# Kernel tuning notes

Hardware: AMD Instinct MI355X
Metric: run time of the kernel (lower is better)

Reference implementation:

```python
import jax, jax.numpy as jnp
import numpy as np

RES = 32            # input grid resolution
OUT_RES = 64        # after subdivide
C = 128             # channels (== out_channels -> skip is identity)
G = 32              # group-norm groups
N = 8192            # active input voxels
EPS = 1e-5

# 8 child offsets for subdivide, 27 stencil offsets for 3x3x3 submanifold conv
_OFFS8 = np.stack(np.meshgrid([0, 1], [0, 1], [0, 1], indexing='ij'), -1).reshape(-1, 3).astype(np.int32)
_OFFS27 = np.stack(np.meshgrid([-1, 0, 1], [-1, 0, 1], [-1, 0, 1], indexing='ij'), -1).reshape(-1, 3).astype(np.int32)


def group_norm(x, gamma, beta, num_groups=G, eps=EPS):
    # sparse group norm over all active voxels of the (single) sample
    n, c = x.shape
    xg = x.reshape(n, num_groups, c // num_groups)
    mean = xg.mean(axis=(0, 2), keepdims=True)
    var = xg.var(axis=(0, 2), keepdims=True)
    xn = (xg - mean) * jax.lax.rsqrt(var + eps)
    return xn.reshape(n, c) * gamma + beta


def subdivide_coords(coords):
    offs = jnp.asarray(_OFFS8)
    return (coords[:, None, :] * 2 + offs[None, :, :]).reshape(-1, 3)  # [8N, 3]


def subm_conv3d(feats, coords, W, b, grid_res):
    # submanifold 3x3x3 sparse conv: outputs only at active sites
    n = feats.shape[0]
    grid = jnp.full((grid_res, grid_res, grid_res), -1, dtype=jnp.int32)
    grid = grid.at[coords[:, 0], coords[:, 1], coords[:, 2]].set(
        jnp.arange(n, dtype=jnp.int32))
    out = jnp.zeros((n, W.shape[-1]), dtype=feats.dtype)
    for k in range(27):  # fixed small stencil loop
        off = jnp.asarray(_OFFS27[k])
        nb = coords + off
        inb = jnp.all((nb >= 0) & (nb < grid_res), axis=1)
        nbc = jnp.clip(nb, 0, grid_res - 1)
        idx = grid[nbc[:, 0], nbc[:, 1], nbc[:, 2]]
        mask = inb & (idx >= 0)
        g = jnp.where(mask[:, None], feats[jnp.where(mask, idx, 0)], 0.0)
        out = out + g @ W[k]
    return out + b


def setup_inputs() -> dict:
    key = jax.random.key(0)
    ks = jax.random.split(key, 8)
    rng = np.random.default_rng(0)
    flat = rng.choice(RES ** 3, size=N, replace=False)
    coords = np.stack([flat // (RES * RES), (flat // RES) % RES, flat % RES],
                      axis=-1).astype(np.int32)
    feats = jax.random.normal(ks[0], (N, C), dtype=jnp.float32)
    gamma1 = 1.0 + 0.1 * jax.random.normal(ks[1], (C,), dtype=jnp.float32)
    beta1 = 0.1 * jax.random.normal(ks[2], (C,), dtype=jnp.float32)
    W1 = jax.random.normal(ks[3], (27, C, C), dtype=jnp.float32) * 0.05
    b1 = jax.random.normal(ks[4], (C,), dtype=jnp.float32) * 0.05
    gamma2 = 1.0 + 0.1 * jax.random.normal(ks[5], (C,), dtype=jnp.float32)
    beta2 = 0.1 * jax.random.normal(ks[6], (C,), dtype=jnp.float32)
    W2 = jax.random.normal(ks[7], (27, C, C), dtype=jnp.float32) * 0.05
    b2 = jax.random.normal(jax.random.fold_in(key, 99), (C,), dtype=jnp.float32) * 0.05
    return {"feats": feats, "gamma1": gamma1, "beta1": beta1, "W1": W1,
            "b1": b1, "gamma2": gamma2, "beta2": beta2, "W2": W2, "b2": b2,
            "coords": jnp.asarray(coords)}


def reference(feats, gamma1, beta1, W1, b1, gamma2, beta2, W2, b2, coords):
    # act_layers: GroupNorm + SiLU at input resolution
    h = jax.nn.silu(group_norm(feats, gamma1, beta1))
    # subdivide both branch and residual (8 children per voxel)
    new_coords = subdivide_coords(coords)          # [8N, 3] in OUT_RES grid
    h = jnp.repeat(h, 8, axis=0)
    x_sub = jnp.repeat(feats, 8, axis=0)
    # out_layers: conv3 -> GN -> SiLU -> conv3 (submanifold, same active set)
    h = subm_conv3d(h, new_coords, W1, b1, OUT_RES)
    h = jax.nn.silu(group_norm(h, gamma2, beta2))
    h = subm_conv3d(h, new_coords, W2, b2, OUT_RES)
    # skip_connection is Identity since out_channels == channels
    return h + x_sub
```

## Files before the change

### kernel.cpp

```cpp
#include <hip/hip_runtime.h>

#define NPAR   8192
#define NCH    65536
#define RES    32
#define EPS    1e-5f

typedef __attribute__((ext_vector_type(8))) short short8;
typedef __attribute__((ext_vector_type(4))) float floatx4;

__device__ __forceinline__ unsigned short f2bf(float f) {
    union { float f; unsigned u; } v; v.f = f;
    unsigned r = v.u + 0x7fffu + ((v.u >> 16) & 1u);
    return (unsigned short)(r >> 16);
}
__device__ __forceinline__ float bf2f(unsigned short b) {
    union { unsigned u; float f; } v; v.u = ((unsigned)b) << 16;
    return v.f;
}
__device__ __forceinline__ void glds16(const void* g, void* l) {
    __builtin_amdgcn_global_load_lds(
        (__attribute__((address_space(1))) const void*)g,
        (__attribute__((address_space(3))) void*)l, 16, 0, 0);
}
__device__ __forceinline__ int k27_of(int o, int s) {
    return (((o >> 2) & 1) + ((s >> 2) & 1)) * 9 +
           (((o >> 1) & 1) + ((s >> 1) & 1)) * 3 +
           ((o & 1) + (s & 1));
}
__device__ __forceinline__ void axis_dlist(int o, int s, int* d, int& n) {
    if (o == 0) { if (s == 0) { d[0] = -1; n = 1; } else { d[0] = 0; d[1] = 1; n = 2; } }
    else        { if (s == 0) { d[0] = -1; d[1] = 0; n = 2; } else { d[0] = 1; n = 1; } }
}

__global__ void k1_kernel(const int* __restrict__ coords, int* __restrict__ grid32,
                          const float* __restrict__ x, float* __restrict__ sum,
                          float* __restrict__ sq) {
    int b = blockIdx.x;
    int t = threadIdx.x;
    if (b < 32) {
        int p = b * 256 + t;
        grid32[(coords[p*3] << 10) + (coords[p*3+1] << 5) + coords[p*3+2]] = p;
    } else {
        __shared__ float s_sum[32], s_sq[32];
        if (t < 32) { s_sum[t] = 0.0f; s_sq[t] = 0.0f; }
        __syncthreads();
        const float4* x4 = (const float4*)x;
        int total = NPAR * 32;
        int idx0 = (b - 32) * 256 + t;
        int g = idx0 & 31;
        float ls = 0.0f, lq = 0.0f;
        for (int idx = idx0; idx < total; idx += 256 * 256) {
            float4 v = x4[idx];
            ls += v.x + v.y + v.z + v.w;
            lq += v.x * v.x + v.y * v.y + v.z * v.z + v.w * v.w;
        }
        atomicAdd(&s_sum[g], ls);
        atomicAdd(&s_sq[g], lq);
        __syncthreads();
        if (t < 32) { atomicAdd(&sum[t], s_sum[t]); atomicAdd(&sq[t], s_sq[t]); }
    }
}

__global__ void k2_kernel(const int* __restrict__ coords, const int* __restrict__ grid32,
                          int* __restrict__ idx_tab, int* __restrict__ pidx27,
                          const float* __restrict__ W1, const float* __restrict__ W2,
                          unsigned short* __restrict__ Wc1f, unsigned short* __restrict__ Wp2,
                          const float* __restrict__ x, const float* __restrict__ sum,
                          const float* __restrict__ sq, const float* __restrict__ gamma,
                          const float* __restrict__ beta, unsigned short* __restrict__ y) {
    int b = blockIdx.x;
    if (b < 32) {
        int p = b * 256 + threadIdx.x;
        int cx = coords[p*3], cy = coords[p*3+1], cz = coords[p*3+2];
        int r27[27];
#pragma unroll
        for (int k = 0; k < 27; ++k) {
            int nx = cx + k / 9 - 1, ny = cy + (k / 3) % 3 - 1, nz = cz + k % 3 - 1;
            int r = -1;
            if ((unsigned)nx < 32u && (unsigned)ny < 32u && (unsigned)nz < 32u) {
                int g = grid32[(nx << 10) + (ny << 5) + nz];
                if ((unsigned)g < (unsigned)NPAR) r = g;
            }
            r27[k] = r;
            pidx27[k * NPAR + p] = r;
        }
#pragma unroll
        for (int k = 0; k < 27; ++k) {
            const int dx = k / 9 - 1, dy = (k / 3) % 3 - 1, dz = k % 3 - 1;
            int v[8];
#pragma unroll
            for (int o = 0; o < 8; ++o) {
                const int ex = ((o >> 2) & 1) + dx;
                const int ey = ((o >> 1) & 1) + dy;
                const int ez = (o & 1) + dz;
                const int ptap = ((ex >> 1) + 1) * 9 + ((ey >> 1) + 1) * 3 + ((ez >> 1) + 1);
                const int slot = ((ex & 1) << 2) + ((ey & 1) << 1) + (ez & 1);
                int r = r27[ptap];
                v[o] = (r >= 0) ? slot * NPAR + r : -1;
            }
            int4* dst = (int4*)&idx_tab[k * NCH + p * 8];
            dst[0] = make_int4(v[0], v[1], v[2], v[3]);
            dst[1] = make_int4(v[4], v[5], v[6], v[7]);
        }
    } else if (b < 248) {
        int rem = (b - 32) * 256 + threadIdx.x;
        int lane = rem & 63;
        int ks   = (rem >> 6) & 3;
        int nb   = (rem >> 8) & 7;
        int tap  = rem >> 11;
        int n  = nb * 16 + (lane & 15);
        int k0 = ks * 32 + (lane >> 4) * 8;
        unsigned short v[8];
#pragma unroll
        for (int j = 0; j < 8; ++j) v[j] = f2bf(W2[tap * 16384 + (k0 + j) * 128 + n]);
        uint4 pk;
        pk.x = (unsigned)v[0] | ((unsigned)v[1] << 16);
        pk.y = (unsigned)v[2] | ((unsigned)v[3] << 16);
        pk.z = (unsigned)v[4] | ((unsigned)v[5] << 16);
        pk.w = (unsigned)v[6] | ((unsigned)v[7] << 16);
        *(uint4*)&Wp2[(long)rem * 8] = pk;
    } else if (b < 760) {
        int rem = (b - 248) * 256 + threadIdx.x;
        int lane  = rem & 63;
        int ks    = (rem >> 6) & 3;
        int nb    = (rem >> 8) & 7;
        int combo = rem >> 11;
        int o = combo >> 3, s = combo & 7;
        int n  = nb * 16 + (lane & 15);
        int k0 = ks * 32 + (lane >> 4) * 8;
        int d0[2], d1[2], d2[2], n0, n1, n2;
        axis_dlist((o >> 2) & 1, (s >> 2) & 1, d0, n0);
        axis_dlist((o >> 1) & 1, (s >> 1) & 1, d1, n1);
        axis_dlist(o & 1,        s & 1,        d2, n2);
        unsigned short v[8];
#pragma unroll
        for (int j = 0; j < 8; ++j) {
            float acc = 0.0f;
            for (int a = 0; a < n0; ++a)
                for (int bb = 0; bb < n1; ++bb)
                    for (int cc = 0; cc < n2; ++cc) {
                        int kk = (d0[a] + 1) * 9 + (d1[bb] + 1) * 3 + (d2[cc] + 1);
                        acc += W1[kk * 16384 + (k0 + j) * 128 + n];
                    }
            v[j] = f2bf(acc);
        }
        uint4 pk;
        pk.x = (unsigned)v[0] | ((unsigned)v[1] << 16);
        pk.y = (unsigned)v[2] | ((unsigned)v[3] << 16);
        pk.z = (unsigned)v[4] | ((unsigned)v[5] << 16);
        pk.w = (unsigned)v[6] | ((unsigned)v[7] << 16);
        *(uint4*)&Wc1f[(long)rem * 8] = pk;
    } else {
        const float4* x4 = (const float4*)x;
        uint2* y2 = (uint2*)y;
        const float4* g4 = (const float4*)gamma;
        const float4* b4 = (const float4*)beta;
        float cnt = (float)NPAR * 4.0f;
        int total = NPAR * 32;
        for (int idx = (b - 760) * 256 + threadIdx.x; idx < total; idx += 256 * 256) {
            int c4 = idx & 31;
            float mean = sum[c4] / cnt;
            float var = sq[c4] / cnt - mean * mean;
            float rstd = rsqrtf(var + EPS);
            float4 v = x4[idx];
            float4 gm = g4[c4];
            float4 bt = b4[c4];
            float a[4] = {v.x, v.y, v.z, v.w};
            float gg[4] = {gm.x, gm.y, gm.z, gm.w};
            float bb[4] = {bt.x, bt.y, bt.z, bt.w};
            unsigned short o[4];
#pragma unroll
            for (int i = 0; i < 4; ++i) {
                float tv = (a[i] - mean) * rstd * gg[i] + bb[i];
                o[i] = f2bf(tv / (1.0f + __expf(-tv)));
            }
            uint2 pk;
            pk.x = (unsigned)o[0] | ((unsigned)o[1] << 16);
            pk.y = (unsigned)o[2] | ((unsigned)o[3] << 16);
            y2[idx] = pk;
        }
    }
}

__global__ void gn_apply_bf16_kernel(unsigned short* __restrict__ x,
                                     const float* __restrict__ sum, const float* __restrict__ sq,
                                     const float* __restrict__ gamma, const float* __restrict__ beta,
                                     int nrows) {
    uint2* x2 = (uint2*)x;
    const float4* g4 = (const float4*)gamma;
    const float4* b4 = (const float4*)beta;
    float cnt = (float)nrows * 4.0f;
    int total = nrows * 32;
    for (int idx = blockIdx.x * blockDim.x + threadIdx.x; idx < total;
         idx += gridDim.x * blockDim.x) {
        int c4 = idx & 31;
        float mean = sum[c4] / cnt;
        float var = sq[c4] / cnt - mean * mean;
        float rstd = rsqrtf(var + EPS);
        uint2 pk = x2[idx];
        float a[4] = {bf2f((unsigned short)(pk.x & 0xffff)), bf2f((unsigned short)(pk.x >> 16)),
                      bf2f((unsigned short)(pk.y & 0xffff)), bf2f((unsigned short)(pk.y >> 16))};
        float4 gm = g4[c4];
        float4 bt = b4[c4];
        float gg[4] = {gm.x, gm.y, gm.z, gm.w};
        float bb[4] = {bt.x, bt.y, bt.z, bt.w};
        unsigned short o[4];
#pragma unroll
        for (int i = 0; i < 4; ++i) {
            float tv = (a[i] - mean) * rstd * gg[i] + bb[i];
            o[i] = f2bf(tv / (1.0f + __expf(-tv)));
        }
        pk.x = (unsigned)o[0] | ((unsigned)o[1] << 16);
        pk.y = (unsigned)o[2] | ((unsigned)o[3] << 16);
        x2[idx] = pk;
    }
}

__device__ __forceinline__ void mfma_phase(
    const unsigned short* __restrict__ Abuf, short8 (&bfr)[2][4],
    floatx4 (&acc)[8][2], int aswz) {
#pragma unroll
    for (int ks = 0; ks < 4; ++ks) {
        short8 afr[8];
#pragma unroll
        for (int mt = 0; mt < 8; ++mt)
            afr[mt] = *(const short8*)&Abuf[(mt << 11) + (ks << 9) + aswz];
#pragma unroll
        for (int mt = 0; mt < 8; ++mt)
#pragma unroll
            for (int nt = 0; nt < 2; ++nt)
                acc[mt][nt] = __builtin_amdgcn_mfma_f32_16x16x32_bf16(
                    afr[mt], bfr[nt][ks], acc[mt][nt], 0, 0, 0);
    }
}
__device__ __forceinline__ void loadB(const unsigned short* __restrict__ Wtap,
                                      short8 (&bfr)[2][4], int wn, int lane) {
#pragma unroll
    for (int nt = 0; nt < 2; ++nt)
#pragma unroll
        for (int ks = 0; ks < 4; ++ks)
            bfr[nt][ks] = *(const short8*)&Wtap[(((wn * 2 + nt) << 2) + ks) * 512 + (lane << 3)];
}
__device__ __forceinline__ void stageA(const unsigned short* __restrict__ Ag,
                                       int iv0, int iv1, const unsigned short* zsrc,
                                       unsigned short* __restrict__ buf,
                                       int base0, int base1, int cchOff) {
    const unsigned short* g0 = (iv0 >= 0) ? Ag + (long)iv0 * 128 : zsrc;
    const unsigned short* g1 = (iv1 >= 0) ? Ag + (long)iv1 * 128 : zsrc;
#pragma unroll
    for (int i = 0; i < 4; ++i) glds16(g0 + i * 32 + cchOff, &buf[base0 + i * 512]);
#pragma unroll
    for (int i = 0; i < 4; ++i) glds16(g1 + i * 32 + cchOff, &buf[base1 + i * 512]);
}

__global__ void __launch_bounds__(256, 2) conv1_fold_kernel(
    const unsigned short* __restrict__ Ag, const unsigned short* __restrict__ Wc1f,
    const float* __restrict__ bias, const int* __restrict__ pidx27,
    unsigned short* __restrict__ outp, const float* __restrict__ zpage,
    float* __restrict__ gsum, float* __restrict__ gsq) {
    __shared__ unsigned short A_lds[2][16384];

    int t = threadIdx.x;
    int o  = blockIdx.x & 7;
    int P0 = (blockIdx.x >> 3) << 7;
    const unsigned short* Wb = Wc1f + ((long)o << 17);
    int wv = t >> 6, lane = t & 63, quad = lane >> 4, l16 = lane & 15;
    int wn = wv;
    int r16 = lane >> 2, cch = lane & 3;
    int c0 = wv * 2, c1 = wv * 2 + 1;
    int row0 = ((c0 >> 2) << 6) + ((c0 & 3) << 4) + r16;
    int row1 = ((c1 >> 2) << 6) + ((c1 & 3) << 4) + r16;
    int base0 = ((c0 >> 2) << 13) + ((c0 & 3) << 11);
    int base1 = ((c1 >> 2) << 13) + ((c1 & 3) << 11);
    int cchOff = (cch ^ ((r16 >> 1) & 3)) << 3;
    int aswz = (l16 << 5) + ((quad ^ ((l16 >> 1) & 3)) << 3);
    const unsigned short* zsrc = (const unsigned short*)zpage;

    floatx4 acc[8][2];
#pragma unroll
    for (int mt = 0; mt < 8; ++mt)
#pragma unroll
        for (int nt = 0; nt < 2; ++nt)
            acc[mt][nt] = (floatx4){0.f, 0.f, 0.f, 0.f};
    short8 bA[2][4], bB[2][4];

    stageA(Ag, pidx27[k27_of(o, 0) * NPAR + P0 + row0],
               pidx27[k27_of(o, 0) * NPAR + P0 + row1], zsrc, A_lds[0], base0, base1, cchOff);
    loadB(Wb, bA, wn, lane);
    int nv0 = pidx27[k27_of(o, 1) * NPAR + P0 + row0];
    int nv1 = pidx27[k27_of(o, 1) * NPAR + P0 + row1];
    __syncthreads();

#pragma unroll 1
    for (int s = 0; s < 8; s += 2) {
        stageA(Ag, nv0, nv1, zsrc, A_lds[1], base0, base1, cchOff);
        loadB(Wb + ((long)(s + 1) << 14), bB, wn, lane);
        if (s + 2 < 8) {
            nv0 = pidx27[k27_of(o, s + 2) * NPAR + P0 + row0];
            nv1 = pidx27[k27_of(o, s + 2) * NPAR + P0 + row1];
        }
        mfma_phase(A_lds[0], bA, acc, aswz);
        __syncthreads();
        if (s + 2 < 8) {
            stageA(Ag, nv0, nv1, zsrc, A_lds[0], base0, base1, cchOff);
            loadB(Wb + ((long)(s + 2) << 14), bA, wn, lane);
            if (s + 3 < 8) {
                nv0 = pidx27[k27_of(o, s + 3) * NPAR + P0 + row0];
                nv1 = pidx27[k27_of(o, s + 3) * NPAR + P0 + row1];
            }
        }
        mfma_phase(A_lds[1], bB, acc, aswz);
        __syncthreads();
    }

    float s_[2] = {0.f, 0.f}, q_[2] = {0.f, 0.f};
#pragma unroll
    for (int nt = 0; nt < 2; ++nt) {
        int col = wn * 32 + nt * 16 + l16;
        float bv = bias[col];
#pragma unroll
        for (int mt = 0; mt < 8; ++mt) {
#pragma unroll
            for (int r = 0; r < 4; ++r) {
                int prow = mt * 16 + quad * 4 + r;
                long R = (long)o * NPAR + P0 + prow;
                float v = acc[mt][nt][r] + bv;
                unsigned short u = f2bf(v);
                outp[R * 128 + col] = u;
                float vr = bf2f(u);
                s_[nt] += vr;
                q_[nt] += vr * vr;
            }
        }
    }
    float* sred = (float*)A_lds;
    if (t < 64) sred[t] = 0.0f;
    __syncthreads();
#pragma unroll
    for (int nt = 0; nt < 2; ++nt) {
        int g = (wn * 32 + nt * 16 + l16) >> 2;
        atomicAdd(&sred[g], s_[nt]);
        atomicAdd(&sred[32 + g], q_[nt]);
    }
    __syncthreads();
    if (t < 32) { atomicAdd(&gsum[t], sred[t]); atomicAdd(&gsq[t], sred[32 + t]); }
}

__global__ void __launch_bounds__(256, 2) conv2_kernel(
    const unsigned short* __restrict__ Ag, const unsigned short* __restrict__ Wp,
    const float* __restrict__ bias, const int* __restrict__ idx_tab,
    const float* __restrict__ resid, float* __restrict__ outp,
    const float* __restrict__ zpage) {
    __shared__ unsigned short A_lds[2][16384];

    int t = threadIdx.x;
    int R0 = blockIdx.x * 128;
    int wv = t >> 6, lane = t & 63, quad = lane >> 4, l16 = lane & 15;
    int wn = wv;
    int r16 = lane >> 2, cch = lane & 3;
    int c0 = wv * 2, c1 = wv * 2 + 1;
    int row0 = ((c0 >> 2) << 6) + ((c0 & 3) << 4) + r16;
    int row1 = ((c1 >> 2) << 6) + ((c1 & 3) << 4) + r16;
    int base0 = ((c0 >> 2) << 13) + ((c0 & 3) << 11);
    int base1 = ((c1 >> 2) << 13) + ((c1 & 3) << 11);
    int cchOff = (cch ^ ((r16 >> 1) & 3)) << 3;
    int aswz = (l16 << 5) + ((quad ^ ((l16 >> 1) & 3)) << 3);
    const unsigned short* zsrc = (const unsigned short*)zpage;

    floatx4 acc[8][2];
#pragma unroll
    for (int mt = 0; mt < 8; ++mt)
#pragma unroll
        for (int nt = 0; nt < 2; ++nt)
            acc[mt][nt] = (floatx4){0.f, 0.f, 0.f, 0.f};
    short8 bA[2][4], bB[2][4];

    stageA(Ag, idx_tab[R0 + row0], idx_tab[R0 + row1], zsrc, A_lds[0], base0, base1, cchOff);
    loadB(Wp, bA, wn, lane);
    int nv0 = idx_tab[NCH + R0 + row0], nv1 = idx_tab[NCH + R0 + row1];
    __syncthreads();

#pragma unroll 1
    for (int k = 0; k < 27; k += 2) {
        if (k + 1 < 27) {
            stageA(Ag, nv0, nv1, zsrc, A_lds[1], base0, base1, cchOff);
            loadB(Wp + ((long)(k + 1) << 14), bB, wn, lane);
            if (k + 2 < 27) {
                nv0 = idx_tab[(k + 2) * NCH + R0 + row0];
                nv1 = idx_tab[(k + 2) * NCH + R0 + row1];
            }
        }
        mfma_phase(A_lds[0], bA, acc, aswz);
        __syncthreads();
        if (k + 1 < 27) {
            if (k + 2 < 27) {
                stageA(Ag, nv0, nv1, zsrc, A_lds[0], base0, base1, cchOff);
                loadB(Wp + ((long)(k + 2) << 14), bA, wn, lane);
                if (k + 3 < 27) {
                    nv0 = idx_tab[(k + 3) * NCH + R0 + row0];
                    nv1 = idx_tab[(k + 3) * NCH + R0 + row1];
                }
            }
            mfma_phase(A_lds[1], bB, acc, aswz);
            __syncthreads();
        }
    }

#pragma unroll
    for (int nt = 0; nt < 2; ++nt) {
        int col = wn * 32 + nt * 16 + l16;
        float bv = bias[col];
#pragma unroll
        for (int mt = 0; mt < 8; ++mt) {
#pragma unroll
            for (int r = 0; r < 4; ++r) {
                int row = mt * 16 + quad * 4 + r;
                long R = (long)R0 + row;
                float v = acc[mt][nt][r] + bv + resid[(R >> 3) * 128 + col];
                outp[R * 128 + col] = v;
            }
        }
    }
}

extern "C" void kernel_launch(void* const* d_in, const int* in_sizes, int n_in,
                              void* d_out, int out_size, void* d_ws, size_t ws_size,
                              hipStream_t stream) {
    const float* feats  = (const float*)d_in[0];
    const float* gamma1 = (const float*)d_in[1];
    const float* beta1  = (const float*)d_in[2];
    const float* W1     = (const float*)d_in[3];
    const float* b1     = (const float*)d_in[4];
    const float* gamma2 = (const float*)d_in[5];
    const float* beta2  = (const float*)d_in[6];
    const float* W2     = (const float*)d_in[7];
    const float* b2     = (const float*)d_in[8];
    const int*   coords = (const int*)d_in[9];
    float* out = (float*)d_out;

    char* ws = (char*)d_ws;
    unsigned short* h0b  = (unsigned short*)(ws);
    unsigned short* h1b  = (unsigned short*)(ws + (2u << 20));
    unsigned short* Wc1f = (unsigned short*)(ws + (18u << 20));
    unsigned short* Wp2  = (unsigned short*)(ws + (20u << 20));
    int*   grid32        = (int*)  (ws + (21u << 20));
    float* stats         = (float*)(ws + (21u << 20) + 131072);
    float* zpage         = (float*)(ws + (21u << 20) + 131072 + 512);
    int*   idx_tab       = (int*)  (ws + (22u << 20));
    int*   pidx27        = (int*)  (ws + (30u << 20));

    hipMemsetAsync(stats, 0, 1024, stream);

    k1_kernel<<<288, 256, 0, stream>>>(coords, grid32, feats, stats + 0, stats + 32);
    k2_kernel<<<1016, 256, 0, stream>>>(coords, grid32, idx_tab, pidx27,
                                        W1, W2, Wc1f, Wp2,
                                        feats, stats + 0, stats + 32, gamma1, beta1, h0b);

    conv1_fold_kernel<<<8 * (NPAR / 128), 256, 0, stream>>>(h0b, Wc1f, b1, pidx27,
                                                            h1b, zpage,
                                                            stats + 64, stats + 96);

    gn_apply_bf16_kernel<<<1024, 256, 0, stream>>>(h1b, stats + 64, stats + 96, gamma2, beta2, NCH);

    conv2_kernel<<<NCH / 128, 256, 0, stream>>>(h1b, Wp2, b2, idx_tab,
                                                feats, out, zpage);
}
```

Before: 201.7 us.

## Stage conv epilogues through LDS for coalesced stores; rebalance prep kernels

Both conv epilogues now write their accumulator tiles into swizzled shared memory and then store full rows with 16-byte vector writes, instead of scattered per-element global stores. The weight repacking work moves from the second prep kernel into the first (alongside grid build and stats), and the second kernel keeps only neighbor-table build and GN apply, so the larger kernel is split more evenly. This aims to cut uncoalesced store traffic. The cost is an extra LDS round trip and a barrier per tile.

```diff
diff --git a/kernel.cpp b/kernel.cpp
--- a/kernel.cpp
+++ b/kernel.cpp
@@ -34,76 +34,16 @@
 
 __global__ void k1_kernel(const int* __restrict__ coords, int* __restrict__ grid32,
                           const float* __restrict__ x, float* __restrict__ sum,
-                          float* __restrict__ sq) {
+                          float* __restrict__ sq,
+                          const float* __restrict__ W1, const float* __restrict__ W2,
+                          unsigned short* __restrict__ Wc1f, unsigned short* __restrict__ Wp2) {
     int b = blockIdx.x;
     int t = threadIdx.x;
     if (b < 32) {
         int p = b * 256 + t;
         grid32[(coords[p*3] << 10) + (coords[p*3+1] << 5) + coords[p*3+2]] = p;
-    } else {
-        __shared__ float s_sum[32], s_sq[32];
-        if (t < 32) { s_sum[t] = 0.0f; s_sq[t] = 0.0f; }
-        __syncthreads();
-        const float4* x4 = (const float4*)x;
-        int total = NPAR * 32;
-        int idx0 = (b - 32) * 256 + t;
-        int g = idx0 & 31;
-        float ls = 0.0f, lq = 0.0f;
-        for (int idx = idx0; idx < total; idx += 256 * 256) {
-            float4 v = x4[idx];
-            ls += v.x + v.y + v.z + v.w;
-            lq += v.x * v.x + v.y * v.y + v.z * v.z + v.w * v.w;
-        }
-        atomicAdd(&s_sum[g], ls);
-        atomicAdd(&s_sq[g], lq);
-        __syncthreads();
-        if (t < 32) { atomicAdd(&sum[t], s_sum[t]); atomicAdd(&sq[t], s_sq[t]); }
-    }
-}
-
-__global__ void k2_kernel(const int* __restrict__ coords, const int* __restrict__ grid32,
-                          int* __restrict__ idx_tab, int* __restrict__ pidx27,
-                          const float* __restrict__ W1, const float* __restrict__ W2,
-                          unsigned short* __restrict__ Wc1f, unsigned short* __restrict__ Wp2,
-                          const float* __restrict__ x, const float* __restrict__ sum,
-                          const float* __restrict__ sq, const float* __restrict__ gamma,
-                          const float* __restrict__ beta, unsigned short* __restrict__ y) {
-    int b = blockIdx.x;
-    if (b < 32) {
-        int p = b * 256 + threadIdx.x;
-        int cx = coords[p*3], cy = coords[p*3+1], cz = coords[p*3+2];
-        int r27[27];
-#pragma unroll
-        for (int k = 0; k < 27; ++k) {
-            int nx = cx + k / 9 - 1, ny = cy + (k / 3) % 3 - 1, nz = cz + k % 3 - 1;
-            int r = -1;
-            if ((unsigned)nx < 32u && (unsigned)ny < 32u && (unsigned)nz < 32u) {
-                int g = grid32[(nx << 10) + (ny << 5) + nz];
-                if ((unsigned)g < (unsigned)NPAR) r = g;
-            }
-            r27[k] = r;
-            pidx27[k * NPAR + p] = r;
-        }
-#pragma unroll
-        for (int k = 0; k < 27; ++k) {
-            const int dx = k / 9 - 1, dy = (k / 3) % 3 - 1, dz = k % 3 - 1;
-            int v[8];
-#pragma unroll
-            for (int o = 0; o < 8; ++o) {
-                const int ex = ((o >> 2) & 1) + dx;
-                const int ey = ((o >> 1) & 1) + dy;
-                const int ez = (o & 1) + dz;
-                const int ptap = ((ex >> 1) + 1) * 9 + ((ey >> 1) + 1) * 3 + ((ez >> 1) + 1);
-                const int slot = ((ex & 1) << 2) + ((ey & 1) << 1) + (ez & 1);
-                int r = r27[ptap];
-                v[o] = (r >= 0) ? slot * NPAR + r : -1;
-            }
-            int4* dst = (int4*)&idx_tab[k * NCH + p * 8];
-            dst[0] = make_int4(v[0], v[1], v[2], v[3]);
-            dst[1] = make_int4(v[4], v[5], v[6], v[7]);
-        }
     } else if (b < 248) {
-        int rem = (b - 32) * 256 + threadIdx.x;
+        int rem = (b - 32) * 256 + t;
         int lane = rem & 63;
         int ks   = (rem >> 6) & 3;
         int nb   = (rem >> 8) & 7;
@@ -120,7 +60,7 @@
         pk.w = (unsigned)v[6] | ((unsigned)v[7] << 16);
         *(uint4*)&Wp2[(long)rem * 8] = pk;
     } else if (b < 760) {
-        int rem = (b - 248) * 256 + threadIdx.x;
+        int rem = (b - 248) * 256 + t;
         int lane  = rem & 63;
         int ks    = (rem >> 6) & 3;
         int nb    = (rem >> 8) & 7;
@@ -151,13 +91,73 @@
         pk.w = (unsigned)v[6] | ((unsigned)v[7] << 16);
         *(uint4*)&Wc1f[(long)rem * 8] = pk;
     } else {
+        __shared__ float s_sum[32], s_sq[32];
+        if (t < 32) { s_sum[t] = 0.0f; s_sq[t] = 0.0f; }
+        __syncthreads();
+        const float4* x4 = (const float4*)x;
+        int total = NPAR * 32;
+        int idx0 = (b - 760) * 256 + t;
+        int g = idx0 & 31;
+        float ls = 0.0f, lq = 0.0f;
+        for (int idx = idx0; idx < total; idx += 256 * 256) {
+            float4 v = x4[idx];
+            ls += v.x + v.y + v.z + v.w;
+            lq += v.x * v.x + v.y * v.y + v.z * v.z + v.w * v.w;
+        }
+        atomicAdd(&s_sum[g], ls);
+        atomicAdd(&s_sq[g], lq);
+        __syncthreads();
+        if (t < 32) { atomicAdd(&sum[t], s_sum[t]); atomicAdd(&sq[t], s_sq[t]); }
+    }
+}
+
+__global__ void k2_kernel(const int* __restrict__ coords, const int* __restrict__ grid32,
+                          int* __restrict__ idx_tab, int* __restrict__ pidx27,
+                          const float* __restrict__ x, const float* __restrict__ sum,
+                          const float* __restrict__ sq, const float* __restrict__ gamma,
+                          const float* __restrict__ beta, unsigned short* __restrict__ y) {
+    int b = blockIdx.x;
+    if (b < 32) {
+        int p = b * 256 + threadIdx.x;
+        int cx = coords[p*3], cy = coords[p*3+1], cz = coords[p*3+2];
+        int r27[27];
+#pragma unroll
+        for (int k = 0; k < 27; ++k) {
+            int nx = cx + k / 9 - 1, ny = cy + (k / 3) % 3 - 1, nz = cz + k % 3 - 1;
+            int r = -1;
+            if ((unsigned)nx < 32u && (unsigned)ny < 32u && (unsigned)nz < 32u) {
+                int g = grid32[(nx << 10) + (ny << 5) + nz];
+                if ((unsigned)g < (unsigned)NPAR) r = g;
+            }
+            r27[k] = r;
+            pidx27[k * NPAR + p] = r;
+        }
+#pragma unroll
+        for (int k = 0; k < 27; ++k) {
+            const int dx = k / 9 - 1, dy = (k / 3) % 3 - 1, dz = k % 3 - 1;
+            int v[8];
+#pragma unroll
+            for (int o = 0; o < 8; ++o) {
+                const int ex = ((o >> 2) & 1) + dx;
+                const int ey = ((o >> 1) & 1) + dy;
+                const int ez = (o & 1) + dz;
+                const int ptap = ((ex >> 1) + 1) * 9 + ((ey >> 1) + 1) * 3 + ((ez >> 1) + 1);
+                const int slot = ((ex & 1) << 2) + ((ey & 1) << 1) + (ez & 1);
+                int r = r27[ptap];
+                v[o] = (r >= 0) ? slot * NPAR + r : -1;
+            }
+            int4* dst = (int4*)&idx_tab[k * NCH + p * 8];
+            dst[0] = make_int4(v[0], v[1], v[2], v[3]);
+            dst[1] = make_int4(v[4], v[5], v[6], v[7]);
+        }
+    } else {
         const float4* x4 = (const float4*)x;
         uint2* y2 = (uint2*)y;
         const float4* g4 = (const float4*)gamma;
         const float4* b4 = (const float4*)beta;
         float cnt = (float)NPAR * 4.0f;
         int total = NPAR * 32;
-        for (int idx = (b - 760) * 256 + threadIdx.x; idx < total; idx += 256 * 256) {
+        for (int idx = (b - 32) * 256 + threadIdx.x; idx < total; idx += 256 * 256) {
             int c4 = idx & 31;
             float mean = sum[c4] / cnt;
             float var = sq[c4] / cnt - mean * mean;
@@ -313,6 +313,8 @@
         __syncthreads();
     }
 
+    unsigned short* lds_s = (unsigned short*)A_lds;
+    float* sred = (float*)(&A_lds[1][0]);
     float s_[2] = {0.f, 0.f}, q_[2] = {0.f, 0.f};
 #pragma unroll
     for (int nt = 0; nt < 2; ++nt) {
@@ -322,20 +324,26 @@
         for (int mt = 0; mt < 8; ++mt) {
 #pragma unroll
             for (int r = 0; r < 4; ++r) {
-                int prow = mt * 16 + quad * 4 + r;
-                long R = (long)o * NPAR + P0 + prow;
+                int row = mt * 16 + quad * 4 + r;
                 float v = acc[mt][nt][r] + bv;
                 unsigned short u = f2bf(v);
-                outp[R * 128 + col] = u;
+                lds_s[row * 128 + (col ^ (quad << 4))] = u;
                 float vr = bf2f(u);
                 s_[nt] += vr;
                 q_[nt] += vr * vr;
             }
         }
     }
-    float* sred = (float*)A_lds;
     if (t < 64) sred[t] = 0.0f;
     __syncthreads();
+#pragma unroll
+    for (int it = 0; it < 8; ++it) {
+        int f = it * 256 + t;
+        int row = f >> 4, c = (f & 15) * 8;
+        int sw = ((row >> 2) & 3) << 4;
+        uint4 v = *(const uint4*)&lds_s[row * 128 + (c ^ sw)];
+        *(uint4*)&outp[((long)o * NPAR + P0 + row) * 128 + c] = v;
+    }
 #pragma unroll
     for (int nt = 0; nt < 2; ++nt) {
         int g = (wn * 32 + nt * 16 + l16) >> 2;
@@ -406,6 +414,7 @@
         }
     }
 
+    float* lds_f = (float*)A_lds;
 #pragma unroll
     for (int nt = 0; nt < 2; ++nt) {
         int col = wn * 32 + nt * 16 + l16;
@@ -417,9 +426,18 @@
                 int row = mt * 16 + quad * 4 + r;
                 long R = (long)R0 + row;
                 float v = acc[mt][nt][r] + bv + resid[(R >> 3) * 128 + col];
-                outp[R * 128 + col] = v;
-            }
-        }
+                lds_f[row * 128 + (col ^ (quad << 4))] = v;
+            }
+        }
+    }
+    __syncthreads();
+#pragma unroll
+    for (int it = 0; it < 16; ++it) {
+        int f = it * 256 + t;
+        int row = f >> 5, c = (f & 31) * 4;
+        int sw = ((row >> 2) & 3) << 4;
+        float4 v = *(const float4*)&lds_f[row * 128 + (c ^ sw)];
+        *(float4*)&outp[((long)R0 + row) * 128 + c] = v;
     }
 }
 
@@ -451,10 +469,10 @@
 
     hipMemsetAsync(stats, 0, 1024, stream);
 
-    k1_kernel<<<288, 256, 0, stream>>>(coords, grid32, feats, stats + 0, stats + 32);
-    k2_kernel<<<1016, 256, 0, stream>>>(coords, grid32, idx_tab, pidx27,
-                                        W1, W2, Wc1f, Wp2,
-                                        feats, stats + 0, stats + 32, gamma1, beta1, h0b);
+    k1_kernel<<<1016, 256, 0, stream>>>(coords, grid32, feats, stats + 0, stats + 32,
+                                        W1, W2, Wc1f, Wp2);
+    k2_kernel<<<288, 256, 0, stream>>>(coords, grid32, idx_tab, pidx27,
+                                       feats, stats + 0, stats + 32, gamma1, beta1, h0b);
 
     conv1_fold_kernel<<<8 * (NPAR / 128), 256, 0, stream>>>(h0b, Wc1f, b1, pidx27,
                                                             h1b, zpage,
```

After: 202.4 us. Within noise of the previous version (+0.3%).
